# Kernel optimization log

Hardware: AMD Instinct MI355X
Metric: run time of the kernel (lower is better)

The kernel has to match this reference:

```python
import jax, jax.numpy as jnp
import numpy as np

N, E = 10000, 320000          # nodes, edges
NF, EF = 128, 64              # raw node / edge feat dims
HN, HE = 256, 256             # hidden node / edge dims
NO, EO = 128, 64              # decoder out dims
ITERS = 3


def _w(k, shape):
    # Linear/GRU weight init scaled by fan_in
    return jax.random.normal(k, shape, jnp.float32) / np.sqrt(shape[-1])


def setup_inputs() -> dict:
    key = jax.random.key(0)
    ks = jax.random.split(key, 12)
    return dict(
        nf=jax.random.normal(ks[0], (N, NF), jnp.float32),
        ef=jax.random.normal(ks[1], (E, EF), jnp.float32),
        src=jax.random.randint(ks[2], (E,), 0, N),
        dst=jax.random.randint(ks[3], (E,), 0, N),
        # encoders
        Wne=_w(ks[4], (HN, NF)), bne=jnp.zeros((HN,), jnp.float32),
        Wee=_w(ks[5], (HE, EF)), bee=jnp.zeros((HE,), jnp.float32),
        # edge GRUCell: input = concat(h_src, h_dst) -> 2*HN
        Wih_e=_w(ks[6], (3 * HE, 2 * HN)), Whh_e=_w(ks[7], (3 * HE, HE)),
        bih_e=jnp.zeros((3 * HE,), jnp.float32), bhh_e=jnp.zeros((3 * HE,), jnp.float32),
        # node GRUCell: input = aggregated edge messages -> HE
        Wih_n=_w(ks[8], (3 * HN, HE)), Whh_n=_w(ks[9], (3 * HN, HN)),
        bih_n=jnp.zeros((3 * HN,), jnp.float32), bhh_n=jnp.zeros((3 * HN,), jnp.float32),
        # decoders (MLP with num_neurons=[] == single Linear)
        Wnd=_w(ks[10], (NO, HN)), bnd=jnp.zeros((NO,), jnp.float32),
        Wed=_w(ks[11], (EO, HE)), bed=jnp.zeros((EO,), jnp.float32),
    )


def _gru(x, h, Wih, Whh, bih, bhh):
    # torch.nn.GRUCell math
    gi = x @ Wih.T + bih
    gh = h @ Whh.T + bhh
    ir, iz, inn = jnp.split(gi, 3, axis=-1)
    hr, hz, hn = jnp.split(gh, 3, axis=-1)
    r = jax.nn.sigmoid(ir + hr)
    z = jax.nn.sigmoid(iz + hz)
    n = jnp.tanh(inn + r * hn)
    return (1.0 - z) * n + z * h


def reference(nf, ef, src, dst, Wne, bne, Wee, bee,
              Wih_e, Whh_e, bih_e, bhh_e,
              Wih_n, Whh_n, bih_n, bhh_n,
              Wnd, bnd, Wed, bed):
    # encode
    unf = nf @ Wne.T + bne   # [N, HN]
    uef = ef @ Wee.T + bee   # [E, HE]
    # GRUMPNN: iterative GRU-based message passing
    for _ in range(ITERS):
        xe = jnp.concatenate([unf[src], unf[dst]], axis=-1)      # [E, 2*HN]
        uef = _gru(xe, uef, Wih_e, Whh_e, bih_e, bhh_e)           # edge update
        agg = jax.ops.segment_sum(uef, dst, num_segments=N)       # [N, HE]
        unf = _gru(agg, unf, Wih_n, Whh_n, bih_n, bhh_n)          # node update
    # decode
    return unf @ Wnd.T + bnd, uef @ Wed.T + bed
```

## Files before the change

### kernel.cpp

```cpp
#include <hip/hip_runtime.h>
#include <hip/hip_bf16.h>
#include <cstddef>

typedef _Float16 f16;
typedef f16 f16x8 __attribute__((ext_vector_type(8)));
typedef f16 f16x4 __attribute__((ext_vector_type(4)));
typedef f16 f16x16 __attribute__((ext_vector_type(16)));
typedef float f32x4 __attribute__((ext_vector_type(4)));

#define NNODES 10000
#define NEDGES 320000

__global__ void pack_b(const float* __restrict__ W, f16* __restrict__ P,
                       int Nout, int K, int ldw, int k0) {
    int idx = blockIdx.x * 256 + threadIdx.x;
    int total = Nout * K;
    if (idx >= total) return;
    int i = idx & 7;
    int l = (idx >> 3) & 63;
    int rest = idx >> 9;
    int NB = Nout >> 4;
    int nb = rest % NB;
    int ks = rest / NB;
    int k = ks * 32 + ((l >> 4) << 3) + i;
    int n = nb * 16 + (l & 15);
    P[idx] = (f16)W[(size_t)n * ldw + k0 + k];
}

template <int AMODE, int OMODE>
__global__ void gemm_bias(const void* __restrict__ A_, const f16* __restrict__ P,
                          const float* __restrict__ bias, void* __restrict__ C_,
                          int M, int Nout, int K) {
    const int lane = threadIdx.x & 63, wave = threadIdx.x >> 6;
    const int wm = wave >> 1, wn = wave & 1;
    const int rb = blockIdx.x * 64 + wm * 32;
    const int cb = blockIdx.y * 64 + wn * 32;
    const int NB = Nout >> 4;
    const int kl = (lane >> 4) << 3;
    int r0 = rb + (lane & 15);
    int r1 = r0 + 16;
    int rc0 = r0 < M ? r0 : M - 1;
    int rc1 = r1 < M ? r1 : M - 1;
    f32x4 acc[2][2] = {};
    for (int ks = 0; ks < (K >> 5); ++ks) {
        int kb = ks * 32 + kl;
        f16x8 a0, a1;
        if constexpr (AMODE == 1) {
            const f16* A = (const f16*)A_;
            a0 = *(const f16x8*)(A + (size_t)rc0 * K + kb);
            a1 = *(const f16x8*)(A + (size_t)rc1 * K + kb);
        } else {
            const float* A = (const float*)A_;
            const float* p0 = A + (size_t)rc0 * K + kb;
            const float* p1 = A + (size_t)rc1 * K + kb;
#pragma unroll
            for (int i = 0; i < 8; ++i) { a0[i] = (f16)p0[i]; a1[i] = (f16)p1[i]; }
        }
#pragma unroll
        for (int nf = 0; nf < 2; ++nf) {
            int nb = (cb >> 4) + nf;
            f16x8 b = *(const f16x8*)(P + (((size_t)ks * NB + nb) * 64 + lane) * 8);
            acc[0][nf] = __builtin_amdgcn_mfma_f32_16x16x32_f16(a0, b, acc[0][nf], 0, 0, 0);
            acc[1][nf] = __builtin_amdgcn_mfma_f32_16x16x32_f16(a1, b, acc[1][nf], 0, 0, 0);
        }
    }
#pragma unroll
    for (int mf = 0; mf < 2; ++mf)
#pragma unroll
        for (int nf = 0; nf < 2; ++nf)
#pragma unroll
            for (int reg = 0; reg < 4; ++reg) {
                int row = rb + mf * 16 + ((lane >> 4) << 2) + reg;
                int col = cb + nf * 16 + (lane & 15);
                if (row < M) {
                    float v = acc[mf][nf][reg] + bias[col];
                    if constexpr (OMODE == 0)
                        ((float*)C_)[(size_t)row * Nout + col] = v;
                    else
                        ((f16*)C_)[(size_t)row * Nout + col] = (f16)v;
                }
            }
}

__global__ void gemm_gi2(const f16* __restrict__ A,
                         const f16* __restrict__ Ps, const f16* __restrict__ Pd,
                         const float* __restrict__ bias,
                         f16* __restrict__ Gs, f16* __restrict__ Gd, int M) {
    const int by = blockIdx.y;
    const bool isD = by >= 12;
    const f16* P = isD ? Pd : Ps;
    f16* G = isD ? Gd : Gs;
    const int byy = isD ? by - 12 : by;
    const int lane = threadIdx.x & 63, wave = threadIdx.x >> 6;
    const int wm = wave >> 1, wn = wave & 1;
    const int rb = blockIdx.x * 64 + wm * 32;
    const int cb = byy * 64 + wn * 32;
    const int NB = 48;
    const int kl = (lane >> 4) << 3;
    int r0 = rb + (lane & 15);
    int r1 = r0 + 16;
    int rc0 = r0 < M ? r0 : M - 1;
    int rc1 = r1 < M ? r1 : M - 1;
    f32x4 acc[2][2] = {};
    for (int ks = 0; ks < 8; ++ks) {
        int kb = ks * 32 + kl;
        f16x8 a0 = *(const f16x8*)(A + (size_t)rc0 * 256 + kb);
        f16x8 a1 = *(const f16x8*)(A + (size_t)rc1 * 256 + kb);
#pragma unroll
        for (int nf = 0; nf < 2; ++nf) {
            int nb = (cb >> 4) + nf;
            f16x8 b = *(const f16x8*)(P + (((size_t)ks * NB + nb) * 64 + lane) * 8);
            acc[0][nf] = __builtin_amdgcn_mfma_f32_16x16x32_f16(a0, b, acc[0][nf], 0, 0, 0);
            acc[1][nf] = __builtin_amdgcn_mfma_f32_16x16x32_f16(a1, b, acc[1][nf], 0, 0, 0);
        }
    }
#pragma unroll
    for (int mf = 0; mf < 2; ++mf)
#pragma unroll
        for (int nf = 0; nf < 2; ++nf)
#pragma unroll
            for (int reg = 0; reg < 4; ++reg) {
                int row = rb + mf * 16 + ((lane >> 4) << 2) + reg;
                int col = cb + nf * 16 + (lane & 15);
                if (row < M) {
                    float v = acc[mf][nf][reg];
                    if (!isD) v += bias[col];
                    G[(size_t)row * 1024 + (col & 255) * 4 + (col >> 8)] = (f16)v;
                }
            }
}

__device__ inline float sigmoidf_(float x) {
    return __fdividef(1.f, 1.f + __expf(-x));
}
__device__ inline float tanhf_(float x) {
    float t = __expf(2.f * x);
    return 1.f - __fdividef(2.f, t + 1.f);
}

__global__ __launch_bounds__(1024, 4) void edge_gru(
        const f16* __restrict__ Gs, const f16* __restrict__ Gd,
        f16* __restrict__ uef,
        const int* __restrict__ src, const int* __restrict__ dst,
        const int* __restrict__ eidx,
        const f16* __restrict__ Phh, const float* __restrict__ bhh,
        float* __restrict__ agg) {
    __shared__ int s_eid[64];
    __shared__ int s_src[64];
    __shared__ int s_dst[64];
    __shared__ char lds_h[64 * 528];
    const int t = threadIdx.x;
    const int p0 = blockIdx.x * 64;
    if (t < 64) {
        int e = eidx[p0 + t];
        s_eid[t] = e;
        s_src[t] = src[e];
        s_dst[t] = dst[e];
    }
#pragma unroll
    for (int i = 0; i < 2; ++i) {
        int s = t + i * 1024;
        int row = s >> 5, seg = s & 31;
        int e = eidx[p0 + row];
        f16x8 v = *(const f16x8*)(uef + (size_t)e * 256 + seg * 8);
        *(f16x8*)(lds_h + row * 528 + seg * 16) = v;
    }
    __syncthreads();
    const int lane = t & 63;
    const int wv = t >> 6;
    const int klb = (lane >> 4) << 4;
    const int erow = lane & 15;
    f32x4 acc[3][4] = {};
#pragma unroll
    for (int ks = 0; ks < 8; ++ks) {
        f16x8 b[4];
#pragma unroll
        for (int eg = 0; eg < 4; ++eg)
            b[eg] = *(const f16x8*)(lds_h + (eg * 16 + erow) * 528 + ks * 64 + klb);
#pragma unroll
        for (int g = 0; g < 3; ++g) {
            f16x8 a = *(const f16x8*)(Phh + (size_t)g * 65536
                                      + (((size_t)ks * 16 + wv) * 64 + lane) * 8);
#pragma unroll
            for (int eg = 0; eg < 4; ++eg)
                acc[g][eg] = __builtin_amdgcn_mfma_f32_16x16x32_f16(a, b[eg], acc[g][eg], 0, 0, 0);
        }
    }
    __syncthreads();
    {
        const int j0 = wv * 16 + ((lane >> 4) << 2);
        const f32x4 bhr = *(const f32x4*)(bhh + j0);
        const f32x4 bhz = *(const f32x4*)(bhh + 256 + j0);
        const f32x4 bhn = *(const f32x4*)(bhh + 512 + j0);
#pragma unroll
        for (int eg = 0; eg < 4; ++eg) {
            const int rr = eg * 16 + erow;
            const int sn = s_src[rr], dn = s_dst[rr];
            f16x16 gsv = *(const f16x16*)(Gs + (size_t)sn * 1024 + j0 * 4);
            f16x16 gdv = *(const f16x16*)(Gd + (size_t)dn * 1024 + j0 * 4);
            f16x4 hv = *(const f16x4*)(lds_h + rr * 528 + j0 * 2);
            f16x4 outv;
#pragma unroll
            for (int q = 0; q < 4; ++q) {
                float ir = (float)gsv[q * 4 + 0] + (float)gdv[q * 4 + 0];
                float iz = (float)gsv[q * 4 + 1] + (float)gdv[q * 4 + 1];
                float in = (float)gsv[q * 4 + 2] + (float)gdv[q * 4 + 2];
                float r = sigmoidf_(ir + acc[0][eg][q] + bhr[q]);
                float z = sigmoidf_(iz + acc[1][eg][q] + bhz[q]);
                float nn = tanhf_(in + r * (acc[2][eg][q] + bhn[q]));
                float h = (float)hv[q];
                outv[q] = (f16)(nn + z * (h - nn));
            }
            *(f16x4*)(lds_h + rr * 528 + j0 * 2) = outv;
        }
    }
    __syncthreads();
#pragma unroll
    for (int i = 0; i < 2; ++i) {
        int s = t + i * 1024;
        int row = s >> 5, seg = s & 31;
        f16x8 v = *(const f16x8*)(lds_h + row * 528 + seg * 16);
        *(f16x8*)(uef + (size_t)s_eid[row] * 256 + seg * 8) = v;
    }
    {
        const int c = t & 255;
        const int q = t >> 8;
        float a = 0.f;
        int d = s_dst[q * 16];
#pragma unroll
        for (int r = q * 16; r < q * 16 + 16; ++r) {
            a += (float)*(const f16*)(lds_h + r * 528 + c * 2);
            int dn = (r < 63) ? s_dst[r + 1] : -1;
            if (r == q * 16 + 15 || dn != d) {
                atomicAdd(&agg[(size_t)d * 256 + c], a);
                a = 0.f;
                d = dn;
            }
        }
    }
}

__global__ __launch_bounds__(1024) void node_gru(
        const float* __restrict__ agg, f16* __restrict__ unf16,
        const f16* __restrict__ Pih, const f16* __restrict__ Phh,
        const float* __restrict__ bih, const float* __restrict__ bhh, int M) {
    const int lane = threadIdx.x & 63, wave = threadIdx.x >> 6;
    const int wm = wave & 1, wn = wave >> 1;
    const int rb = blockIdx.x * 64 + wm * 32;
    const int cb = wn * 32;
    const int nb0 = wn * 2;
    const int kl = (lane >> 4) << 3;
    int r0 = rb + (lane & 15), r1 = r0 + 16;
    int rc0 = r0 < M ? r0 : M - 1;
    int rc1 = r1 < M ? r1 : M - 1;
    f32x4 acc[4][2][2] = {};
#pragma unroll
    for (int ks = 0; ks < 8; ++ks) {
        const float* p0 = agg + (size_t)rc0 * 256 + ks * 32 + kl;
        const float* p1 = agg + (size_t)rc1 * 256 + ks * 32 + kl;
        f16x8 a0, a1;
#pragma unroll
        for (int i = 0; i < 8; ++i) { a0[i] = (f16)p0[i]; a1[i] = (f16)p1[i]; }
#pragma unroll
        for (int g = 0; g < 3; ++g) {
            const f16* Pg = Pih + (size_t)g * (256 * 256);
#pragma unroll
            for (int nf = 0; nf < 2; ++nf) {
                f16x8 b = *(const f16x8*)(Pg + (((size_t)ks * 16 + nb0 + nf) * 64 + lane) * 8);
                acc[g][0][nf] = __builtin_amdgcn_mfma_f32_16x16x32_f16(a0, b, acc[g][0][nf], 0, 0, 0);
                acc[g][1][nf] = __builtin_amdgcn_mfma_f32_16x16x32_f16(a1, b, acc[g][1][nf], 0, 0, 0);
            }
        }
    }
#pragma unroll
    for (int ks = 0; ks < 8; ++ks) {
        f16x8 a0 = *(const f16x8*)(unf16 + (size_t)rc0 * 256 + ks * 32 + kl);
        f16x8 a1 = *(const f16x8*)(unf16 + (size_t)rc1 * 256 + ks * 32 + kl);
#pragma unroll
        for (int g = 0; g < 3; ++g) {
            const f16* Pg = Phh + (size_t)g * (256 * 256);
            const int tgt = (g == 2) ? 3 : g;
#pragma unroll
            for (int nf = 0; nf < 2; ++nf) {
                f16x8 b = *(const f16x8*)(Pg + (((size_t)ks * 16 + nb0 + nf) * 64 + lane) * 8);
                acc[tgt][0][nf] = __builtin_amdgcn_mfma_f32_16x16x32_f16(a0, b, acc[tgt][0][nf], 0, 0, 0);
                acc[tgt][1][nf] = __builtin_amdgcn_mfma_f32_16x16x32_f16(a1, b, acc[tgt][1][nf], 0, 0, 0);
            }
        }
    }
    __syncthreads();
#pragma unroll
    for (int mf = 0; mf < 2; ++mf) {
        const int row = rb + mf * 16 + ((lane >> 4) << 2);
#pragma unroll
        for (int nf = 0; nf < 2; ++nf) {
            const int j = cb + nf * 16 + (lane & 15);
            const float b_r = bih[j] + bhh[j];
            const float b_z = bih[256 + j] + bhh[256 + j];
            const float b_i = bih[512 + j];
            const float b_h = bhh[512 + j];
#pragma unroll
            for (int reg = 0; reg < 4; ++reg) {
                const int rr = row + reg;
                if (rr < M) {
                    float r = sigmoidf_(acc[0][mf][nf][reg] + b_r);
                    float z = sigmoidf_(acc[1][mf][nf][reg] + b_z);
                    float nn = tanhf_(acc[2][mf][nf][reg] + b_i + r * (acc[3][mf][nf][reg] + b_h));
                    float h = (float)unf16[(size_t)rr * 256 + j];
                    unf16[(size_t)rr * 256 + j] = (f16)(nn + z * (h - nn));
                }
            }
        }
    }
}

__global__ void hist_k(const int* __restrict__ dst, int* __restrict__ cnt, int E) {
    int e = blockIdx.x * 256 + threadIdx.x;
    if (e < E) atomicAdd(&cnt[dst[e]], 1);
}

__global__ void scan_k(const int* __restrict__ cnt, int* __restrict__ rowptr, int n) {
    __shared__ int s[1024];
    __shared__ int carry_s;
    if (threadIdx.x == 0) { carry_s = 0; rowptr[0] = 0; }
    __syncthreads();
    for (int base = 0; base < n; base += 1024) {
        int i = base + (int)threadIdx.x;
        int v = (i < n) ? cnt[i] : 0;
        s[threadIdx.x] = v;
        __syncthreads();
        for (int off = 1; off < 1024; off <<= 1) {
            int tv = (threadIdx.x >= (unsigned)off) ? s[threadIdx.x - off] : 0;
            __syncthreads();
            s[threadIdx.x] += tv;
            __syncthreads();
        }
        if (i < n) rowptr[i + 1] = carry_s + s[threadIdx.x];
        __syncthreads();
        if (threadIdx.x == 0) carry_s += s[1023];
        __syncthreads();
    }
}

__global__ void scatter_k(const int* __restrict__ dst, const int* __restrict__ rowptr,
                          int* __restrict__ cnt2, int* __restrict__ eidx, int E) {
    int e = blockIdx.x * 256 + threadIdx.x;
    if (e < E) {
        int d = dst[e];
        int p = rowptr[d] + atomicAdd(&cnt2[d], 1);
        eidx[p] = e;
    }
}

extern "C" void kernel_launch(void* const* d_in, const int* in_sizes, int n_in,
                              void* d_out, int out_size, void* d_ws, size_t ws_size,
                              hipStream_t stream) {
    (void)in_sizes; (void)n_in; (void)out_size; (void)ws_size;
    const float* nf    = (const float*)d_in[0];
    const float* ef    = (const float*)d_in[1];
    const int*   src   = (const int*)d_in[2];
    const int*   dst   = (const int*)d_in[3];
    const float* Wne   = (const float*)d_in[4];
    const float* bne   = (const float*)d_in[5];
    const float* Wee   = (const float*)d_in[6];
    const float* bee   = (const float*)d_in[7];
    const float* Wih_e = (const float*)d_in[8];
    const float* Whh_e = (const float*)d_in[9];
    const float* bih_e = (const float*)d_in[10];
    const float* bhh_e = (const float*)d_in[11];
    const float* Wih_n = (const float*)d_in[12];
    const float* Whh_n = (const float*)d_in[13];
    const float* bih_n = (const float*)d_in[14];
    const float* bhh_n = (const float*)d_in[15];
    const float* Wnd   = (const float*)d_in[16];
    const float* bnd   = (const float*)d_in[17];
    const float* Wed   = (const float*)d_in[18];
    const float* bed   = (const float*)d_in[19];

    char* ws = (char*)d_ws;
    size_t off = 0;
    auto alloc = [&](size_t bytes) -> void* {
        void* p = ws + off;
        off += (bytes + 255) & ~(size_t)255;
        return p;
    };
    f16*   uefA  = (f16*)alloc((size_t)NEDGES * 256 * 2);
    f16*   unf16 = (f16*)alloc((size_t)NNODES * 256 * 2);
    float* agg   = (float*)alloc((size_t)NNODES * 256 * 4);
    f16*   Gs    = (f16*)alloc((size_t)NNODES * 1024 * 2);
    f16*   Gd    = (f16*)alloc((size_t)NNODES * 1024 * 2);
    f16*   Ps_e  = (f16*)alloc((size_t)768 * 256 * 2);
    f16*   Pd_e  = (f16*)alloc((size_t)768 * 256 * 2);
    f16*   Phh_e = (f16*)alloc((size_t)3 * 256 * 256 * 2);
    f16*   Pih_n = (f16*)alloc((size_t)3 * 256 * 256 * 2);
    f16*   Phh_n = (f16*)alloc((size_t)3 * 256 * 256 * 2);
    f16*   Pne   = (f16*)alloc((size_t)256 * 128 * 2);
    f16*   Pee   = (f16*)alloc((size_t)256 * 64 * 2);
    f16*   Pnd   = (f16*)alloc((size_t)128 * 256 * 2);
    f16*   Ped   = (f16*)alloc((size_t)64 * 256 * 2);
    int* cnt    = (int*)alloc((size_t)NNODES * 4);
    int* cnt2   = (int*)alloc((size_t)NNODES * 4);
    int* rowptr = (int*)alloc((size_t)(NNODES + 1) * 4);
    int* eidx   = (int*)alloc((size_t)NEDGES * 4);

    hipMemsetAsync(cnt, 0, (size_t)NNODES * 4, stream);
    hipMemsetAsync(cnt2, 0, (size_t)NNODES * 4, stream);

    pack_b<<<(768 * 256 + 255) / 256, 256, 0, stream>>>(Wih_e, Ps_e, 768, 256, 512, 0);
    pack_b<<<(768 * 256 + 255) / 256, 256, 0, stream>>>(Wih_e, Pd_e, 768, 256, 512, 256);
    for (int g = 0; g < 3; ++g) {
        pack_b<<<(256 * 256 + 255) / 256, 256, 0, stream>>>(Whh_e + (size_t)g * 256 * 256,
                                                            Phh_e + (size_t)g * 256 * 256, 256, 256, 256, 0);
        pack_b<<<(256 * 256 + 255) / 256, 256, 0, stream>>>(Wih_n + (size_t)g * 256 * 256,
                                                            Pih_n + (size_t)g * 256 * 256, 256, 256, 256, 0);
        pack_b<<<(256 * 256 + 255) / 256, 256, 0, stream>>>(Whh_n + (size_t)g * 256 * 256,
                                                            Phh_n + (size_t)g * 256 * 256, 256, 256, 256, 0);
    }
    pack_b<<<(256 * 128 + 255) / 256, 256, 0, stream>>>(Wne, Pne, 256, 128, 128, 0);
    pack_b<<<(256 * 64 + 255) / 256, 256, 0, stream>>>(Wee, Pee, 256, 64, 64, 0);
    pack_b<<<(128 * 256 + 255) / 256, 256, 0, stream>>>(Wnd, Pnd, 128, 256, 256, 0);
    pack_b<<<(64 * 256 + 255) / 256, 256, 0, stream>>>(Wed, Ped, 64, 256, 256, 0);

    hist_k<<<(NEDGES + 255) / 256, 256, 0, stream>>>(dst, cnt, NEDGES);
    scan_k<<<1, 1024, 0, stream>>>(cnt, rowptr, NNODES);
    scatter_k<<<(NEDGES + 255) / 256, 256, 0, stream>>>(dst, rowptr, cnt2, eidx, NEDGES);

    gemm_bias<0, 1><<<dim3(157, 4), 256, 0, stream>>>(nf, Pne, bne, unf16, NNODES, 256, 128);
    gemm_bias<0, 1><<<dim3(5000, 4), 256, 0, stream>>>(ef, Pee, bee, uefA, NEDGES, 256, 64);

    for (int it = 0; it < 3; ++it) {
        gemm_gi2<<<dim3(157, 24), 256, 0, stream>>>(unf16, Ps_e, Pd_e, bih_e, Gs, Gd, NNODES);
        hipMemsetAsync(agg, 0, (size_t)NNODES * 256 * 4, stream);
        edge_gru<<<5000, 1024, 0, stream>>>(Gs, Gd, uefA, src, dst, eidx, Phh_e, bhh_e, agg);
        node_gru<<<157, 1024, 0, stream>>>(agg, unf16, Pih_n, Phh_n, bih_n, bhh_n, NNODES);
    }

    gemm_bias<1, 0><<<dim3(157, 2), 256, 0, stream>>>(unf16, Pnd, bnd, d_out, NNODES, 128, 256);
    gemm_bias<1, 0><<<dim3(5000, 1), 256, 0, stream>>>(uefA, Ped, bed,
                                                       (float*)d_out + (size_t)NNODES * 128,
                                                       NEDGES, 64, 256);
}
```

Measured before the change: 1.752 ms.

## Fuse edge-input projection and agg zeroing into node GRU, batch weight packing

The node GRU kernel now stages the updated node states in LDS and, for the first two iterations, computes the next iteration's Gs/Gd edge-input projections in the same kernel. It also zeroes its own rows of the aggregation buffer, replacing the separate per-iteration memset and gemm_gi2 launches. The fifteen separate weight-packing launches become one batched kernel, and the edge GRU adds the Gs and Gd gathers as f16 vectors before converting to float. This removes launches and a re-read of node states, at the cost of extra LDS, a longer node kernel running on only 157 blocks, and the f16 addition losing some precision.

```diff
diff --git a/kernel.cpp b/kernel.cpp
--- a/kernel.cpp
+++ b/kernel.cpp
@@ -11,20 +11,23 @@
 #define NNODES 10000
 #define NEDGES 320000
 
-__global__ void pack_b(const float* __restrict__ W, f16* __restrict__ P,
-                       int Nout, int K, int ldw, int k0) {
+struct PackJob { const float* W; f16* P; int Nout, K, ldw, k0; };
+struct PackJobs { PackJob j[15]; };
+
+__global__ void pack_all(PackJobs jobs) {
+    const PackJob J = jobs.j[blockIdx.y];
     int idx = blockIdx.x * 256 + threadIdx.x;
-    int total = Nout * K;
+    int total = J.Nout * J.K;
     if (idx >= total) return;
     int i = idx & 7;
     int l = (idx >> 3) & 63;
     int rest = idx >> 9;
-    int NB = Nout >> 4;
+    int NB = J.Nout >> 4;
     int nb = rest % NB;
     int ks = rest / NB;
     int k = ks * 32 + ((l >> 4) << 3) + i;
     int n = nb * 16 + (l & 15);
-    P[idx] = (f16)W[(size_t)n * ldw + k0 + k];
+    J.P[idx] = (f16)J.W[(size_t)n * J.ldw + J.k0 + k];
 }
 
 template <int AMODE, int OMODE>
@@ -198,13 +201,14 @@
             const int sn = s_src[rr], dn = s_dst[rr];
             f16x16 gsv = *(const f16x16*)(Gs + (size_t)sn * 1024 + j0 * 4);
             f16x16 gdv = *(const f16x16*)(Gd + (size_t)dn * 1024 + j0 * 4);
+            f16x16 gsum = gsv + gdv;
             f16x4 hv = *(const f16x4*)(lds_h + rr * 528 + j0 * 2);
             f16x4 outv;
 #pragma unroll
             for (int q = 0; q < 4; ++q) {
-                float ir = (float)gsv[q * 4 + 0] + (float)gdv[q * 4 + 0];
-                float iz = (float)gsv[q * 4 + 1] + (float)gdv[q * 4 + 1];
-                float in = (float)gsv[q * 4 + 2] + (float)gdv[q * 4 + 2];
+                float ir = (float)gsum[q * 4 + 0];
+                float iz = (float)gsum[q * 4 + 1];
+                float in = (float)gsum[q * 4 + 2];
                 float r = sigmoidf_(ir + acc[0][eg][q] + bhr[q]);
                 float z = sigmoidf_(iz + acc[1][eg][q] + bhz[q]);
                 float nn = tanhf_(in + r * (acc[2][eg][q] + bhn[q]));
@@ -240,13 +244,19 @@
     }
 }
 
-__global__ __launch_bounds__(1024) void node_gru(
-        const float* __restrict__ agg, f16* __restrict__ unf16,
+__global__ __launch_bounds__(1024) void node_gru_gi(
+        float* __restrict__ agg, f16* __restrict__ unf16,
         const f16* __restrict__ Pih, const f16* __restrict__ Phh,
-        const float* __restrict__ bih, const float* __restrict__ bhh, int M) {
-    const int lane = threadIdx.x & 63, wave = threadIdx.x >> 6;
+        const float* __restrict__ bih, const float* __restrict__ bhh,
+        const f16* __restrict__ Ps, const f16* __restrict__ Pd,
+        const float* __restrict__ bie,
+        f16* __restrict__ Gs, f16* __restrict__ Gd, int M, int doG) {
+    __shared__ char lds_u[64 * 528];
+    const int t = threadIdx.x;
+    const int lane = t & 63, wave = t >> 6;
     const int wm = wave & 1, wn = wave >> 1;
-    const int rb = blockIdx.x * 64 + wm * 32;
+    const int rb0 = blockIdx.x * 64;
+    const int rb = rb0 + wm * 32;
     const int cb = wn * 32;
     const int nb0 = wn * 2;
     const int kl = (lane >> 4) << 3;
@@ -289,9 +299,18 @@
         }
     }
     __syncthreads();
+    {
+        int nrows = M - rb0;
+        if (nrows > 64) nrows = 64;
+        if (nrows > 0) {
+            int totf = nrows * 256;
+            for (int s = t * 4; s < totf; s += 4096)
+                *(f32x4*)(agg + (size_t)rb0 * 256 + s) = f32x4{0.f, 0.f, 0.f, 0.f};
+        }
+    }
 #pragma unroll
     for (int mf = 0; mf < 2; ++mf) {
-        const int row = rb + mf * 16 + ((lane >> 4) << 2);
+        const int lrow = wm * 32 + mf * 16 + ((lane >> 4) << 2);
 #pragma unroll
         for (int nf = 0; nf < 2; ++nf) {
             const int j = cb + nf * 16 + (lane & 15);
@@ -301,16 +320,51 @@
             const float b_h = bhh[512 + j];
 #pragma unroll
             for (int reg = 0; reg < 4; ++reg) {
-                const int rr = row + reg;
-                if (rr < M) {
-                    float r = sigmoidf_(acc[0][mf][nf][reg] + b_r);
-                    float z = sigmoidf_(acc[1][mf][nf][reg] + b_z);
-                    float nn = tanhf_(acc[2][mf][nf][reg] + b_i + r * (acc[3][mf][nf][reg] + b_h));
-                    float h = (float)unf16[(size_t)rr * 256 + j];
-                    unf16[(size_t)rr * 256 + j] = (f16)(nn + z * (h - nn));
-                }
-            }
-        }
+                const int lr = lrow + reg;
+                const int rr = rb0 + lr;
+                float r = sigmoidf_(acc[0][mf][nf][reg] + b_r);
+                float z = sigmoidf_(acc[1][mf][nf][reg] + b_z);
+                float nn = tanhf_(acc[2][mf][nf][reg] + b_i + r * (acc[3][mf][nf][reg] + b_h));
+                float h = (float)unf16[(size_t)(rr < M ? rr : M - 1) * 256 + j];
+                f16 v = (f16)(nn + z * (h - nn));
+                *(f16*)(lds_u + lr * 528 + j * 2) = v;
+                if (rr < M) unf16[(size_t)rr * 256 + j] = v;
+            }
+        }
+    }
+    if (!doG) return;
+    __syncthreads();
+    const int wv = t >> 6;
+    const int klb = (lane >> 4) << 4;
+    const int arow = lane & 15;
+#pragma unroll
+    for (int cgi = 0; cgi < 6; ++cgi) {
+        const int cg = wv * 6 + cgi;
+        const bool isD = cg >= 48;
+        const int nb = isD ? cg - 48 : cg;
+        const f16* P = isD ? Pd : Ps;
+        f16* G = isD ? Gd : Gs;
+        f32x4 a4[4] = {};
+#pragma unroll
+        for (int ks = 0; ks < 8; ++ks) {
+            f16x8 b = *(const f16x8*)(P + (((size_t)ks * 48 + nb) * 64 + lane) * 8);
+#pragma unroll
+            for (int mf = 0; mf < 4; ++mf) {
+                f16x8 a = *(const f16x8*)(lds_u + (mf * 16 + arow) * 528 + ks * 64 + klb);
+                a4[mf] = __builtin_amdgcn_mfma_f32_16x16x32_f16(a, b, a4[mf], 0, 0, 0);
+            }
+        }
+        const int col = nb * 16 + (lane & 15);
+        const float bv = isD ? 0.f : bie[col];
+        const size_t goff = (size_t)(col & 255) * 4 + (col >> 8);
+#pragma unroll
+        for (int mf = 0; mf < 4; ++mf)
+#pragma unroll
+            for (int reg = 0; reg < 4; ++reg) {
+                int grow = rb0 + mf * 16 + ((lane >> 4) << 2) + reg;
+                if (grow < M)
+                    G[(size_t)grow * 1024 + goff] = (f16)(a4[mf][reg] + bv);
+            }
     }
 }
 
@@ -405,21 +459,21 @@
 
     hipMemsetAsync(cnt, 0, (size_t)NNODES * 4, stream);
     hipMemsetAsync(cnt2, 0, (size_t)NNODES * 4, stream);
-
-    pack_b<<<(768 * 256 + 255) / 256, 256, 0, stream>>>(Wih_e, Ps_e, 768, 256, 512, 0);
-    pack_b<<<(768 * 256 + 255) / 256, 256, 0, stream>>>(Wih_e, Pd_e, 768, 256, 512, 256);
+    hipMemsetAsync(agg, 0, (size_t)NNODES * 256 * 4, stream);
+
+    PackJobs jobs;
+    jobs.j[0]  = {Wih_e, Ps_e, 768, 256, 512, 0};
+    jobs.j[1]  = {Wih_e, Pd_e, 768, 256, 512, 256};
     for (int g = 0; g < 3; ++g) {
-        pack_b<<<(256 * 256 + 255) / 256, 256, 0, stream>>>(Whh_e + (size_t)g * 256 * 256,
-                                                            Phh_e + (size_t)g * 256 * 256, 256, 256, 256, 0);
-        pack_b<<<(256 * 256 + 255) / 256, 256, 0, stream>>>(Wih_n + (size_t)g * 256 * 256,
-                                                            Pih_n + (size_t)g * 256 * 256, 256, 256, 256, 0);
-        pack_b<<<(256 * 256 + 255) / 256, 256, 0, stream>>>(Whh_n + (size_t)g * 256 * 256,
-                                                            Phh_n + (size_t)g * 256 * 256, 256, 256, 256, 0);
-    }
-    pack_b<<<(256 * 128 + 255) / 256, 256, 0, stream>>>(Wne, Pne, 256, 128, 128, 0);
-    pack_b<<<(256 * 64 + 255) / 256, 256, 0, stream>>>(Wee, Pee, 256, 64, 64, 0);
-    pack_b<<<(128 * 256 + 255) / 256, 256, 0, stream>>>(Wnd, Pnd, 128, 256, 256, 0);
-    pack_b<<<(64 * 256 + 255) / 256, 256, 0, stream>>>(Wed, Ped, 64, 256, 256, 0);
+        jobs.j[2 + g] = {Whh_e + (size_t)g * 65536, Phh_e + (size_t)g * 65536, 256, 256, 256, 0};
+        jobs.j[5 + g] = {Wih_n + (size_t)g * 65536, Pih_n + (size_t)g * 65536, 256, 256, 256, 0};
+        jobs.j[8 + g] = {Whh_n + (size_t)g * 65536, Phh_n + (size_t)g * 65536, 256, 256, 256, 0};
+    }
+    jobs.j[11] = {Wne, Pne, 256, 128, 128, 0};
+    jobs.j[12] = {Wee, Pee, 256, 64, 64, 0};
+    jobs.j[13] = {Wnd, Pnd, 128, 256, 256, 0};
+    jobs.j[14] = {Wed, Ped, 64, 256, 256, 0};
+    pack_all<<<dim3(768, 15), 256, 0, stream>>>(jobs);
 
     hist_k<<<(NEDGES + 255) / 256, 256, 0, stream>>>(dst, cnt, NEDGES);
     scan_k<<<1, 1024, 0, stream>>>(cnt, rowptr, NNODES);
@@ -428,11 +482,13 @@
     gemm_bias<0, 1><<<dim3(157, 4), 256, 0, stream>>>(nf, Pne, bne, unf16, NNODES, 256, 128);
     gemm_bias<0, 1><<<dim3(5000, 4), 256, 0, stream>>>(ef, Pee, bee, uefA, NEDGES, 256, 64);
 
+    gemm_gi2<<<dim3(157, 24), 256, 0, stream>>>(unf16, Ps_e, Pd_e, bih_e, Gs, Gd, NNODES);
+
     for (int it = 0; it < 3; ++it) {
-        gemm_gi2<<<dim3(157, 24), 256, 0, stream>>>(unf16, Ps_e, Pd_e, bih_e, Gs, Gd, NNODES);
-        hipMemsetAsync(agg, 0, (size_t)NNODES * 256 * 4, stream);
         edge_gru<<<5000, 1024, 0, stream>>>(Gs, Gd, uefA, src, dst, eidx, Phh_e, bhh_e, agg);
-        node_gru<<<157, 1024, 0, stream>>>(agg, unf16, Pih_n, Phh_n, bih_n, bhh_n, NNODES);
+        node_gru_gi<<<157, 1024, 0, stream>>>(agg, unf16, Pih_n, Phh_n, bih_n, bhh_n,
+                                              Ps_e, Pd_e, bih_e, Gs, Gd, NNODES,
+                                              (it < 2) ? 1 : 0);
     }
 
     gemm_bias<1, 0><<<dim3(157, 2), 256, 0, stream>>>(unf16, Pnd, bnd, d_out, NNODES, 128, 256);
```

Result: slower. 2.120 ms (+21.0%).
